# Kernel optimization log

Measured on AMD Instinct MI355X. Metric: run time of the kernel, lower is better.

The kernel has to match this reference:

```python
import jax, jax.numpy as jnp
import numpy as np

N = 1024      # num_waves
L = 32        # latent_dim
H = 64        # hidden_dim
EPS = 1e-6
SELF_SCALE = 0.5
INT_SCALE = 0.3


def _xavier(k, shape, gain=0.5):
    fan_out, fan_in = shape
    std = gain * np.sqrt(2.0 / (fan_in + fan_out))
    return (jax.random.normal(k, shape, jnp.float32) * std).astype(jnp.float32)


def setup_inputs() -> dict:
    key = jax.random.key(0)
    ks = jax.random.split(key, 12)
    d = {}
    d['state'] = jax.random.normal(ks[0], (N * (L + 1),), jnp.float32)
    # SelfDynamicsNetwork: L->H->H->L, tanh, xavier_normal gain=0.5, zero bias
    d['Ws1'] = _xavier(ks[1], (H, L)); d['bs1'] = jnp.zeros((H,), jnp.float32)
    d['Ws2'] = _xavier(ks[2], (H, H)); d['bs2'] = jnp.zeros((H,), jnp.float32)
    d['Ws3'] = _xavier(ks[3], (L, H)); d['bs3'] = jnp.zeros((L,), jnp.float32)
    # InteractionNetwork: 4L->H->H->L
    d['Wi1'] = _xavier(ks[4], (H, 4 * L)); d['bi1'] = jnp.zeros((H,), jnp.float32)
    d['Wi2'] = _xavier(ks[5], (H, H));     d['bi2'] = jnp.zeros((H,), jnp.float32)
    d['Wi3'] = _xavier(ks[6], (L, H));     d['bi3'] = jnp.zeros((L,), jnp.float32)
    # QuantumPhaseMixer
    d['phase_w'] = jax.random.normal(ks[7], (L,), jnp.float32) * 0.1
    d['Wc'] = _xavier(ks[8], (L, 2 * L), gain=1.0)
    d['bc'] = jnp.zeros((L,), jnp.float32)
    # per-wave aggressiveness
    d['aggr'] = jnp.ones((N,), jnp.float32) * 0.5
    return d


def reference(state, Ws1, bs1, Ws2, bs2, Ws3, bs3,
              Wi1, bi1, Wi2, bi2, Wi3, bi3,
              phase_w, Wc, bc, aggr):
    s = state.reshape(N, L + 1)
    h = s[:, :L]          # [N, L]
    phases = s[:, L]      # [N]

    def mlp(x, W1, b1, W2, b2, W3, b3):
        x = jnp.tanh(x @ W1.T + b1)
        x = jnp.tanh(x @ W2.T + b2)
        return x @ W3.T + b3

    self_term = mlp(h, Ws1, bs1, Ws2, bs2, Ws3, bs3)   # [N, L]
    dh = self_term  # prev_state is None -> estimated velocity = self_dynamics(h)

    # pairwise distance factor
    diff = h[:, None, :] - h[None, :, :]                # [N, N, L] (h_i - h_j)
    dist = jnp.linalg.norm(diff, axis=-1) + EPS         # [N, N]
    dfac = jnp.minimum(1.0 / dist, 2.0)

    # InteractionNetwork on concat([h_i, h_j, dh_i, dh_j]): split first layer
    a_i = h @ Wi1[:, :L].T + dh @ Wi1[:, 2 * L:3 * L].T           # [N, H]
    b_j = h @ Wi1[:, L:2 * L].T + dh @ Wi1[:, 3 * L:].T + bi1    # [N, H]
    x1 = jnp.tanh(a_i[:, None, :] + b_j[None, :, :])              # [N, N, H]
    x2 = jnp.tanh(x1 @ Wi2.T + bi2)                               # [N, N, H]
    k_ij = x2 @ Wi3.T + bi3                                       # [N, N, L]

    # QuantumPhaseMixer
    phase_diff = phases[:, None] - phases[None, :]                # [N, N]
    pf = jnp.cos(phase_diff[..., None] * phase_w)                 # [N, N, L]
    coh = jax.nn.sigmoid((h @ Wc[:, :L].T)[:, None, :]
                         + (h @ Wc[:, L:].T)[None, :, :] + bc)    # [N, N, L]
    quantum = pf * coh * (-diff)                                  # h_j - h_i = -diff

    agg = jax.nn.sigmoid(aggr)                                    # [N]
    inter = dfac[..., None] * k_ij * agg[:, None, None] + quantum # [N, N, L]
    mask = 1.0 - jnp.eye(N, dtype=inter.dtype)                    # skip j == i
    isum = jnp.einsum('ijl,ij->il', inter, mask)                  # sum over j

    # env is None -> speed_mults = 1, refractions = 0
    dh_dt = SELF_SCALE * self_term + INT_SCALE * isum
    dphase = 0.1 + 0.05 * jnp.sum(jnp.abs(isum), axis=-1)
    return jnp.concatenate([dh_dt, dphase[:, None]], axis=1).reshape(-1)
```

## Files before the change

### kernel.cpp

```cpp
#include <hip/hip_runtime.h>
#include <hip/hip_bf16.h>
#include <math.h>

#define NN 1024
#define LDIM 32
#define HDIM 64

#define WS_SELF 0
#define WS_AA   (WS_SELF + NN*LDIM)
#define WS_CI   (WS_AA   + NN*HDIM)
#define WS_AGG  (WS_CI   + NN*LDIM)
#define WS_BI2  (WS_AGG  + NN)
#define WS_BI3  (WS_BI2  + HDIM)
#define WS_FEND (WS_BI3  + LDIM)

#define U_BJB  0
#define U_HJB  (U_BJB + NN*HDIM)
#define U_JT   (U_HJB + NN*LDIM)
#define U_W2B  (U_JT  + NN*LDIM*4)
#define U_W3B  (U_W2B + HDIM*HDIM)
#define U_END  (U_W3B + LDIM*HDIM)

#define PK_W1  0
#define PK_W2  1024
#define PK_W3  3072
#define PK_WI1 4096
#define PK_WC  8192
#define PK_END 9216

#define K2P  2.88539008f
#define K1N  (-1.44269504f)

typedef __attribute__((ext_vector_type(8))) short bf16x8;
typedef __attribute__((ext_vector_type(4))) float f32x4;
typedef __attribute__((ext_vector_type(2))) float v2f;

__device__ __forceinline__ float fast_rcp(float x) { return __builtin_amdgcn_rcpf(x); }
__device__ __forceinline__ float fast_tanh(float x) {
    float e = __builtin_amdgcn_exp2f(x * K2P);
    return 1.0f - 2.0f * fast_rcp(e + 1.0f);
}
__device__ __forceinline__ float fast_sigmoid(float x) {
    return fast_rcp(1.0f + __builtin_amdgcn_exp2f(x * K1N));
}
__device__ __forceinline__ float blo(unsigned int u) { union { unsigned int i; float f; } v; v.i = u << 16; return v.f; }
__device__ __forceinline__ float bhi(unsigned int u) { union { unsigned int i; float f; } v; v.i = u & 0xffff0000u; return v.f; }
__device__ __forceinline__ float bf2f(unsigned short u) { union { unsigned int i; float f; } v; v.i = ((unsigned int)u) << 16; return v.f; }
__device__ __forceinline__ unsigned short f2bf(float f) {
    __hip_bfloat16 b = __float2bfloat16(f);
    unsigned short u; __builtin_memcpy(&u, &b, 2); return u;
}
__device__ __forceinline__ unsigned int pk2(float a, float b) {
    float2 t; t.x = a; t.y = b;
    __hip_bfloat162 h = __float22bfloat162_rn(t);
    unsigned int u; __builtin_memcpy(&u, &h, 4); return u;
}

__device__ __forceinline__ v2f tanh2_fact(v2f ea, v2f eb) {
    v2f d = ea * eb + 1.0f;
    v2f r; r.x = fast_rcp(d.x); r.y = fast_rcp(d.y);
    return 1.0f - 2.0f * r;
}

__global__ __launch_bounds__(256) void precompute(
    const float* __restrict__ state,
    const float* __restrict__ Ws1, const float* __restrict__ bs1,
    const float* __restrict__ Ws2, const float* __restrict__ bs2,
    const float* __restrict__ Ws3, const float* __restrict__ bs3,
    const float* __restrict__ Wi1, const float* __restrict__ bi1,
    const float* __restrict__ Wi2, const float* __restrict__ bi2,
    const float* __restrict__ Wi3, const float* __restrict__ bi3,
    const float* __restrict__ phw, const float* __restrict__ Wc,
    const float* __restrict__ bc,  const float* __restrict__ aggr,
    float* __restrict__ ws, unsigned short* __restrict__ wsu) {
    const int tid = threadIdx.x;
    const int w = tid >> 6, t = tid & 63;
    const int i = blockIdx.x * 4 + w;

    __shared__ unsigned int wlds[PK_END];
    __shared__ float shh[4][32], shdh[4][32], sht1[4][64], sht2[4][64];
    __shared__ float shph[4];

    {
        const float2* s1 = (const float2*)Ws1;
        #pragma unroll
        for (int r = 0; r < 4; r++) { int e = tid + r * 256; int f = e >> 4, k2 = e & 15;
            float2 v = s1[e]; wlds[PK_W1 + k2 * 64 + f] = pk2(v.x, v.y); }
        const float2* s2 = (const float2*)Ws2;
        #pragma unroll
        for (int r = 0; r < 8; r++) { int e = tid + r * 256; int f = e >> 5, k2 = e & 31;
            float2 v = s2[e]; wlds[PK_W2 + k2 * 64 + f] = pk2(v.x, v.y); }
        const float2* s3 = (const float2*)Ws3;
        #pragma unroll
        for (int r = 0; r < 4; r++) { int e = tid + r * 256; int f = e >> 5, k2 = e & 31;
            float2 v = s3[e]; wlds[PK_W3 + k2 * 32 + f] = pk2(v.x, v.y); }
        const float2* si = (const float2*)Wi1;
        #pragma unroll
        for (int r = 0; r < 16; r++) { int e = tid + r * 256; int f = e >> 6, c2 = e & 63;
            float2 v = si[e]; wlds[PK_WI1 + c2 * 64 + f] = pk2(v.x, v.y); }
        const float2* sc = (const float2*)Wc;
        #pragma unroll
        for (int r = 0; r < 4; r++) { int e = tid + r * 256; int f = e >> 5, c2 = e & 31;
            float2 v = sc[e]; wlds[PK_WC + c2 * 32 + f] = pk2(v.x, v.y); }
    }
    if (blockIdx.x == 0) {
        #pragma unroll
        for (int r = 0; r < 16; r++) { int e = tid + r * 256; wsu[U_W2B + e] = f2bf(Wi2[e]); }
        #pragma unroll
        for (int r = 0; r < 8; r++)  { int e = tid + r * 256; wsu[U_W3B + e] = f2bf(Wi3[e]); }
        if (tid < HDIM) ws[WS_BI2 + tid] = bi2[tid];
        if (tid < LDIM) ws[WS_BI3 + tid] = bi3[tid];
    }

    float sv = (t < 33) ? state[i * 33 + t] : 0.f;
    if (t < 32) shh[w][t] = sv;
    if (t == 32) shph[w] = sv;
    if (t == 33) ws[WS_AGG + i] = fast_sigmoid(aggr[i]);
    __syncthreads();

    {
        float s = bs1[t];
        const unsigned int* W = wlds + PK_W1;
        #pragma unroll
        for (int k2 = 0; k2 < 16; k2++) {
            unsigned int p = W[k2 * 64 + t];
            s = fmaf(blo(p), shh[w][2 * k2], s);
            s = fmaf(bhi(p), shh[w][2 * k2 + 1], s);
        }
        sht1[w][t] = fast_tanh(s);
    }
    __syncthreads();
    {
        float s = bs2[t];
        const unsigned int* W = wlds + PK_W2;
        #pragma unroll
        for (int k2 = 0; k2 < 32; k2++) {
            unsigned int p = W[k2 * 64 + t];
            s = fmaf(blo(p), sht1[w][2 * k2], s);
            s = fmaf(bhi(p), sht1[w][2 * k2 + 1], s);
        }
        sht2[w][t] = fast_tanh(s);
    }
    __syncthreads();
    if (t < 32) {
        float s = bs3[t];
        const unsigned int* W = wlds + PK_W3;
        #pragma unroll
        for (int k2 = 0; k2 < 32; k2++) {
            unsigned int p = W[k2 * 32 + t];
            s = fmaf(blo(p), sht2[w][2 * k2], s);
            s = fmaf(bhi(p), sht2[w][2 * k2 + 1], s);
        }
        ws[WS_SELF + i * 32 + t] = s;
        shdh[w][t] = s;
    }
    __syncthreads();
    {
        float sa = 0.f, sb = bi1[t];
        const unsigned int* W = wlds + PK_WI1;
        #pragma unroll
        for (int k2 = 0; k2 < 16; k2++) {
            float h0 = shh[w][2 * k2], h1 = shh[w][2 * k2 + 1];
            float d0 = shdh[w][2 * k2], d1 = shdh[w][2 * k2 + 1];
            unsigned int wa  = W[k2 * 64 + t];
            unsigned int wb  = W[(16 + k2) * 64 + t];
            unsigned int wa2 = W[(32 + k2) * 64 + t];
            unsigned int wb2 = W[(48 + k2) * 64 + t];
            sa = fmaf(blo(wa), h0, sa);  sa = fmaf(bhi(wa), h1, sa);
            sb = fmaf(blo(wb), h0, sb);  sb = fmaf(bhi(wb), h1, sb);
            sa = fmaf(blo(wa2), d0, sa); sa = fmaf(bhi(wa2), d1, sa);
            sb = fmaf(blo(wb2), d0, sb); sb = fmaf(bhi(wb2), d1, sb);
        }
        ws[WS_AA + i * 64 + t]  = __builtin_amdgcn_exp2f(sa * K2P);
        wsu[U_BJB + i * 64 + t] = f2bf(__builtin_amdgcn_exp2f(sb * K2P));
    }
    if (t < 32) {
        float si2 = 0.f, sj = 0.f;
        const unsigned int* W = wlds + PK_WC;
        #pragma unroll
        for (int m2 = 0; m2 < 16; m2++) {
            float h0 = shh[w][2 * m2], h1 = shh[w][2 * m2 + 1];
            unsigned int wi = W[m2 * 32 + t];
            unsigned int wj = W[(16 + m2) * 32 + t];
            si2 = fmaf(blo(wi), h0, si2); si2 = fmaf(bhi(wi), h1, si2);
            sj  = fmaf(blo(wj), h0, sj);  sj  = fmaf(bhi(wj), h1, sj);
        }
        ws[WS_CI + i * 32 + t] = __builtin_amdgcn_exp2f((si2 + bc[t]) * K1N);
        float h = shh[w][t];
        wsu[U_HJB + i * 32 + t] = f2bf(h);
        float ejn = __builtin_amdgcn_exp2f(sj * K1N);
        float sc_, cc_;
        __sincosf(shph[w] * phw[t], &sc_, &cc_);
        int p = (t & 15) + 16;
        float h_p  = __shfl(h,   p);
        float e_p  = __shfl(ejn, p);
        float cc_p = __shfl(cc_, p);
        float sc_p = __shfl(sc_, p);
        if (t < 16) {
            uint4 o; o.x = pk2(h, h_p); o.y = pk2(ejn, e_p);
            o.z = pk2(cc_, cc_p); o.w = pk2(sc_, sc_p);
            *(uint4*)(wsu + U_JT + (i * 16 + t) * 8) = o;
        }
    }
}

__global__ __launch_bounds__(256) void pair_kernel(
    const float* __restrict__ ws, const unsigned short* __restrict__ wsu,
    float* __restrict__ out) {
    const int i    = blockIdx.x;
    const int tid  = threadIdx.x;
    const int w    = tid >> 6;
    const int lane = tid & 63;
    const int q    = lane >> 4;
    const int m    = lane & 15;
    const int jw   = w * 16;
    const int sub  = lane & 3;

    __shared__ unsigned short W2ls[64 * 72];
    __shared__ unsigned short x2ls[4 * 16 * 72];
    __shared__ float redT[4][32], redU[4][32], redV[4][32];
    __shared__ float sfw[4];

    {
        int row = tid >> 2, c = (tid & 3) * 16;
        const uint4* s2 = (const uint4*)(wsu + U_W2B + row * 64 + c);
        uint4 d0 = s2[0], d1 = s2[1];
        uint4* dd = (uint4*)(&W2ls[row * 72 + c]);
        dd[0] = d0; dd[1] = d1;
    }
    bf16x8 w3r[2][2];
    #pragma unroll
    for (int lb = 0; lb < 2; lb++)
        #pragma unroll
        for (int s = 0; s < 2; s++)
            w3r[lb][s] = *(const bf16x8*)(wsu + U_W3B + (lb * 16 + m) * 64 + s * 32 + q * 8);

    v2f hi2[4];
    {
        uint4 hv4 = *(const uint4*)(wsu + U_HJB + i * 32 + sub * 8);
        unsigned int hd[4] = {hv4.x, hv4.y, hv4.z, hv4.w};
        #pragma unroll
        for (int e = 0; e < 4; e++) { hi2[e].x = blo(hd[e]); hi2[e].y = bhi(hd[e]); }
    }
    f32x4 b2q[4];
    #pragma unroll
    for (int nb = 0; nb < 4; nb++) {
        float4 bv = *(const float4*)(ws + WS_BI2 + nb * 16 + q * 4);
        b2q[nb][0] = bv.x; b2q[nb][1] = bv.y; b2q[nb][2] = bv.z; b2q[nb][3] = bv.w;
    }
    v2f ea2[8];
    {
        const float* ap = ws + WS_AA + i * 64 + q * 8;
        #pragma unroll
        for (int s = 0; s < 2; s++) {
            float4 lo = *(const float4*)(ap + s * 32);
            float4 hi = *(const float4*)(ap + s * 32 + 4);
            ea2[s * 4 + 0].x = lo.x; ea2[s * 4 + 0].y = lo.y;
            ea2[s * 4 + 1].x = lo.z; ea2[s * 4 + 1].y = lo.w;
            ea2[s * 4 + 2].x = hi.x; ea2[s * 4 + 2].y = hi.y;
            ea2[s * 4 + 3].x = hi.z; ea2[s * 4 + 3].y = hi.w;
        }
    }
    v2f hiv2, ei2;
    hiv2.x = bf2f(wsu[U_HJB + i * 32 + m]);      hiv2.y = bf2f(wsu[U_HJB + i * 32 + 16 + m]);
    ei2.x = ws[WS_CI + i * 32 + m];              ei2.y = ws[WS_CI + i * 32 + 16 + m];
    const float aggi = ws[WS_AGG + i];
    const float sub0 = (sub == 0) ? 1.0f : 0.0f;

    const unsigned short* hp = wsu + U_HJB + (jw + (lane >> 2)) * 32 + sub * 8;
    const unsigned short* bp = wsu + U_BJB + (jw + m) * 64 + q * 8;
    const unsigned short* jp = wsu + U_JT + ((jw + q * 4) * 16 + m) * 8;

    uint4 hvA = *(const uint4*)hp;
    uint4 b0A = *(const uint4*)bp;
    uint4 b1A = *(const uint4*)(bp + 32);
    uint4 hvB, b0B, b1B;
    __syncthreads();

    f32x4 accK[2];
    #pragma unroll
    for (int lb = 0; lb < 2; lb++) { accK[lb][0]=0.f; accK[lb][1]=0.f; accK[lb][2]=0.f; accK[lb][3]=0.f; }
    v2f u2; u2.x = 0.f; u2.y = 0.f;
    v2f vv2; vv2.x = 0.f; vv2.y = 0.f;
    float sumfac = 0.f;

    unsigned short* xb = &x2ls[w * 1152];

    auto stageB = [&]() {
        bf16x8 x2f[2];
        #pragma unroll
        for (int s = 0; s < 2; s++)
            x2f[s] = *(const bf16x8*)(&xb[m * 72 + s * 32 + q * 8]);
        #pragma unroll
        for (int lb = 0; lb < 2; lb++) {
            #pragma unroll
            for (int s = 0; s < 2; s++) {
                accK[lb] = __builtin_amdgcn_mfma_f32_16x16x32_bf16(x2f[s], w3r[lb][s], accK[lb], 0, 0, 0);
            }
        }
    };

    auto body = [&](int T, const uint4& hvc, const uint4& b0c, const uint4& b1c,
                    uint4& hvn, uint4& b0n, uint4& b1n) {
        hp += 2048; bp += 4096;
        hvn = *(const uint4*)hp;
        b0n = *(const uint4*)bp;
        b1n = *(const uint4*)(bp + 32);

        uint4 jt4[4];
        #pragma unroll
        for (int r = 0; r < 4; r++) jt4[r] = *(const uint4*)(jp + r * 128);
        jp += 8192;

        if (T > 0) stageB();

        float facm;
        {
            unsigned int hd[4] = {hvc.x, hvc.y, hvc.z, hvc.w};
            v2f s2v; s2v.x = 0.f; s2v.y = 0.f;
            #pragma unroll
            for (int e = 0; e < 4; e++) {
                v2f hj; hj.x = blo(hd[e]); hj.y = bhi(hd[e]);
                v2f d = hi2[e] - hj;
                s2v += d * d;
            }
            float s = s2v.x + s2v.y;
            s += __shfl_xor(s, 1); s += __shfl_xor(s, 2);
            int jj = T * 64 + jw + (lane >> 2);
            float facown = fminf(__builtin_amdgcn_rsqf(s), 2.0f) * aggi;
            facown = (jj == i) ? 0.0f : facown;
            sumfac = fmaf(sub0, facown, sumfac);
            facm = __shfl(facown, 4 * m);
        }

        bf16x8 afr[2];
        {
            unsigned int bd[8] = {b0c.x, b0c.y, b0c.z, b0c.w, b1c.x, b1c.y, b1c.z, b1c.w};
            #pragma unroll
            for (int s = 0; s < 2; s++) {
                union { uint4 u4; bf16x8 v; } pkd;
                #pragma unroll
                for (int e = 0; e < 4; e++) {
                    unsigned int bw = bd[s * 4 + e];
                    v2f eb; eb.x = blo(bw); eb.y = bhi(bw);
                    v2f t2 = tanh2_fact(ea2[s * 4 + e], eb);
                    ((unsigned int*)&pkd.u4)[e] = pk2(t2.x, t2.y);
                }
                afr[s] = pkd.v;
            }
        }

        f32x4 accA[4];
        #pragma unroll
        for (int nb = 0; nb < 4; nb++) {
            f32x4 acc = b2q[nb];
            #pragma unroll
            for (int s = 0; s < 2; s++) {
                bf16x8 w2f = *(const bf16x8*)(&W2ls[(nb * 16 + m) * 72 + s * 32 + q * 8]);
                acc = __builtin_amdgcn_mfma_f32_16x16x32_bf16(w2f, afr[s], acc, 0, 0, 0);
            }
            accA[nb] = acc;
        }
        #pragma unroll
        for (int nb = 0; nb < 4; nb++) {
            v2f zA; zA.x = accA[nb][0]; zA.y = accA[nb][1];
            v2f zB; zB.x = accA[nb][2]; zB.y = accA[nb][3];
            v2f zzA = zA * zA, zzB = zB * zB;
            v2f nA = zA * (zzA + 15.0f), nB = zB * (zzB + 15.0f);
            v2f dA = zzA * 6.0f + 15.0f, dB = zzB * 6.0f + 15.0f;
            v2f rA, rB;
            rA.x = fast_rcp(dA.x); rA.y = fast_rcp(dA.y);
            rB.x = fast_rcp(dB.x); rB.y = fast_rcp(dB.y);
            v2f tA = nA * (rA * facm);
            v2f tB = nB * (rB * facm);
            uint2 pk; pk.x = pk2(tA.x, tA.y); pk.y = pk2(tB.x, tB.y);
            *(uint2*)(&xb[m * 72 + nb * 16 + q * 4]) = pk;
        }

        #pragma unroll
        for (int r = 0; r < 4; r++) {
            uint4 jv = jt4[r];
            v2f hj2; hj2.x = blo(jv.x); hj2.y = bhi(jv.x);
            v2f ej2; ej2.x = blo(jv.y); ej2.y = bhi(jv.y);
            v2f pc2; pc2.x = blo(jv.z); pc2.y = bhi(jv.z);
            v2f ps2; ps2.x = blo(jv.w); ps2.y = bhi(jv.w);
            v2f dd = ei2 * ej2 + 1.0f;
            v2f coh; coh.x = fast_rcp(dd.x); coh.y = fast_rcp(dd.y);
            v2f cd = coh * (hiv2 - hj2);
            u2  += cd * pc2;
            vv2 += cd * ps2;
        }
    };

    #pragma unroll 1
    for (int T = 0; T < 16; T += 2) {
        body(T,     hvA, b0A, b1A, hvB, b0B, b1B);
        body(T + 1, hvB, b0B, b1B, hvA, b0A, b1A);
    }
    stageB();

    float T1[2];
    float aU[2] = {u2.x, u2.y};
    float aV[2] = {vv2.x, vv2.y};
    #pragma unroll
    for (int lb = 0; lb < 2; lb++) {
        T1[lb] = (accK[lb][0] + accK[lb][1]) + (accK[lb][2] + accK[lb][3]);
        T1[lb] += __shfl_xor(T1[lb], 16); T1[lb] += __shfl_xor(T1[lb], 32);
        aU[lb] += __shfl_xor(aU[lb], 16); aU[lb] += __shfl_xor(aU[lb], 32);
        aV[lb] += __shfl_xor(aV[lb], 16); aV[lb] += __shfl_xor(aV[lb], 32);
    }
    sumfac += __shfl_xor(sumfac, 1);  sumfac += __shfl_xor(sumfac, 2);
    sumfac += __shfl_xor(sumfac, 4);  sumfac += __shfl_xor(sumfac, 8);
    sumfac += __shfl_xor(sumfac, 16); sumfac += __shfl_xor(sumfac, 32);
    if (lane < 16) {
        redT[w][m] = T1[0];      redT[w][16 + m] = T1[1];
        redU[w][m] = aU[0];      redU[w][16 + m] = aU[1];
        redV[w][m] = aV[0];      redV[w][16 + m] = aV[1];
    }
    if (lane == 0) sfw[w] = sumfac;
    __syncthreads();
    if (tid < 32) {
        int l = tid;
        float t1 = (redT[0][l] + redT[1][l]) + (redT[2][l] + redT[3][l]);
        float uu = (redU[0][l] + redU[1][l]) + (redU[2][l] + redU[3][l]);
        float vvv = (redV[0][l] + redV[1][l]) + (redV[2][l] + redV[3][l]);
        float sf = (sfw[0] + sfw[1]) + (sfw[2] + sfw[3]);
        int mm = l & 15;
        uint2 jti = *(const uint2*)(wsu + U_JT + (i * 16 + mm) * 8 + 4);
        float pic = (l < 16) ? blo(jti.x) : bhi(jti.x);
        float pis = (l < 16) ? blo(jti.y) : bhi(jti.y);
        float isum = t1 + sf * ws[WS_BI3 + l] - (pic * uu + pis * vvv);
        out[i * 33 + l] = 0.5f * ws[WS_SELF + i * 32 + l] + 0.3f * isum;
        float ab = fabsf(isum);
        ab += __shfl_xor(ab, 1); ab += __shfl_xor(ab, 2);
        ab += __shfl_xor(ab, 4); ab += __shfl_xor(ab, 8);
        ab += __shfl_xor(ab, 16);
        if (tid == 0) out[i * 33 + 32] = 0.1f + 0.05f * ab;
    }
}

extern "C" void kernel_launch(void* const* d_in, const int* in_sizes, int n_in,
                              void* d_out, int out_size, void* d_ws, size_t ws_size,
                              hipStream_t stream) {
    const float* state   = (const float*)d_in[0];
    const float* Ws1     = (const float*)d_in[1];
    const float* bs1     = (const float*)d_in[2];
    const float* Ws2     = (const float*)d_in[3];
    const float* bs2     = (const float*)d_in[4];
    const float* Ws3     = (const float*)d_in[5];
    const float* bs3     = (const float*)d_in[6];
    const float* Wi1     = (const float*)d_in[7];
    const float* bi1     = (const float*)d_in[8];
    const float* Wi2     = (const float*)d_in[9];
    const float* bi2     = (const float*)d_in[10];
    const float* Wi3     = (const float*)d_in[11];
    const float* bi3     = (const float*)d_in[12];
    const float* phase_w = (const float*)d_in[13];
    const float* Wc      = (const float*)d_in[14];
    const float* bc      = (const float*)d_in[15];
    const float* aggr    = (const float*)d_in[16];

    float* ws = (float*)d_ws;
    unsigned short* wsu = (unsigned short*)(ws + WS_FEND);
    float* out = (float*)d_out;

    precompute<<<256, 256, 0, stream>>>(state, Ws1, bs1, Ws2, bs2, Ws3, bs3,
                                        Wi1, bi1, Wi2, bi2, Wi3, bi3,
                                        phase_w, Wc, bc, aggr, ws, wsu);
    pair_kernel<<<NN, 256, 0, stream>>>(ws, wsu, out);
}
```

Before: 142.2 us.

## Sum scaled x2 over j before applying Wi3 instead of per-pair MFMA

Uses linearity of the last interaction layer. The dfac-scaled tanh outputs x2 are accumulated over j in registers, and Wi3 is applied once per row i at the end. This removes the per-tile LDS staging of x2, the bf16 packing and the second MFMA stage, and adds a cross-lane and cross-wave reduction plus a small scalar dot product in the epilogue. It also keeps the accumulation in fp32 rather than rounding to bf16 before the final matmul.

```diff
diff --git a/kernel.cpp b/kernel.cpp
--- a/kernel.cpp
+++ b/kernel.cpp
@@ -217,8 +217,8 @@
     const int sub  = lane & 3;
 
     __shared__ unsigned short W2ls[64 * 72];
-    __shared__ unsigned short x2ls[4 * 16 * 72];
-    __shared__ float redT[4][32], redU[4][32], redV[4][32];
+    __shared__ float redY[4][64];
+    __shared__ float redU[4][32], redV[4][32];
     __shared__ float sfw[4];
 
     {
@@ -228,12 +228,6 @@
         uint4* dd = (uint4*)(&W2ls[row * 72 + c]);
         dd[0] = d0; dd[1] = d1;
     }
-    bf16x8 w3r[2][2];
-    #pragma unroll
-    for (int lb = 0; lb < 2; lb++)
-        #pragma unroll
-        for (int s = 0; s < 2; s++)
-            w3r[lb][s] = *(const bf16x8*)(wsu + U_W3B + (lb * 16 + m) * 64 + s * 32 + q * 8);
 
     v2f hi2[4];
     {
@@ -277,28 +271,12 @@
     uint4 hvB, b0B, b1B;
     __syncthreads();
 
-    f32x4 accK[2];
+    v2f y2[8];
     #pragma unroll
-    for (int lb = 0; lb < 2; lb++) { accK[lb][0]=0.f; accK[lb][1]=0.f; accK[lb][2]=0.f; accK[lb][3]=0.f; }
+    for (int k = 0; k < 8; k++) { y2[k].x = 0.f; y2[k].y = 0.f; }
     v2f u2; u2.x = 0.f; u2.y = 0.f;
     v2f vv2; vv2.x = 0.f; vv2.y = 0.f;
     float sumfac = 0.f;
-
-    unsigned short* xb = &x2ls[w * 1152];
-
-    auto stageB = [&]() {
-        bf16x8 x2f[2];
-        #pragma unroll
-        for (int s = 0; s < 2; s++)
-            x2f[s] = *(const bf16x8*)(&xb[m * 72 + s * 32 + q * 8]);
-        #pragma unroll
-        for (int lb = 0; lb < 2; lb++) {
-            #pragma unroll
-            for (int s = 0; s < 2; s++) {
-                accK[lb] = __builtin_amdgcn_mfma_f32_16x16x32_bf16(x2f[s], w3r[lb][s], accK[lb], 0, 0, 0);
-            }
-        }
-    };
 
     auto body = [&](int T, const uint4& hvc, const uint4& b0c, const uint4& b1c,
                     uint4& hvn, uint4& b0n, uint4& b1n) {
@@ -311,8 +289,6 @@
         #pragma unroll
         for (int r = 0; r < 4; r++) jt4[r] = *(const uint4*)(jp + r * 128);
         jp += 8192;
-
-        if (T > 0) stageB();
 
         float facm;
         {
@@ -371,10 +347,8 @@
             v2f rA, rB;
             rA.x = fast_rcp(dA.x); rA.y = fast_rcp(dA.y);
             rB.x = fast_rcp(dB.x); rB.y = fast_rcp(dB.y);
-            v2f tA = nA * (rA * facm);
-            v2f tB = nB * (rB * facm);
-            uint2 pk; pk.x = pk2(tA.x, tA.y); pk.y = pk2(tB.x, tB.y);
-            *(uint2*)(&xb[m * 72 + nb * 16 + q * 4]) = pk;
+            y2[nb * 2 + 0] += nA * (rA * facm);
+            y2[nb * 2 + 1] += nB * (rB * facm);
         }
 
         #pragma unroll
@@ -397,15 +371,30 @@
         body(T,     hvA, b0A, b1A, hvB, b0B, b1B);
         body(T + 1, hvB, b0B, b1B, hvA, b0A, b1A);
     }
-    stageB();
-
-    float T1[2];
+
+    float yv[16];
+    #pragma unroll
+    for (int nb = 0; nb < 4; nb++) {
+        yv[nb * 4 + 0] = y2[nb * 2 + 0].x; yv[nb * 4 + 1] = y2[nb * 2 + 0].y;
+        yv[nb * 4 + 2] = y2[nb * 2 + 1].x; yv[nb * 4 + 3] = y2[nb * 2 + 1].y;
+    }
+    #pragma unroll
+    for (int k = 0; k < 16; k++) {
+        yv[k] += __shfl_xor(yv[k], 1); yv[k] += __shfl_xor(yv[k], 2);
+        yv[k] += __shfl_xor(yv[k], 4); yv[k] += __shfl_xor(yv[k], 8);
+    }
+    if (m == 0) {
+        #pragma unroll
+        for (int nb = 0; nb < 4; nb++) {
+            #pragma unroll
+            for (int e = 0; e < 4; e++)
+                redY[w][nb * 16 + q * 4 + e] = yv[nb * 4 + e];
+        }
+    }
     float aU[2] = {u2.x, u2.y};
     float aV[2] = {vv2.x, vv2.y};
     #pragma unroll
     for (int lb = 0; lb < 2; lb++) {
-        T1[lb] = (accK[lb][0] + accK[lb][1]) + (accK[lb][2] + accK[lb][3]);
-        T1[lb] += __shfl_xor(T1[lb], 16); T1[lb] += __shfl_xor(T1[lb], 32);
         aU[lb] += __shfl_xor(aU[lb], 16); aU[lb] += __shfl_xor(aU[lb], 32);
         aV[lb] += __shfl_xor(aV[lb], 16); aV[lb] += __shfl_xor(aV[lb], 32);
     }
@@ -413,15 +402,30 @@
     sumfac += __shfl_xor(sumfac, 4);  sumfac += __shfl_xor(sumfac, 8);
     sumfac += __shfl_xor(sumfac, 16); sumfac += __shfl_xor(sumfac, 32);
     if (lane < 16) {
-        redT[w][m] = T1[0];      redT[w][16 + m] = T1[1];
         redU[w][m] = aU[0];      redU[w][16 + m] = aU[1];
         redV[w][m] = aV[0];      redV[w][16 + m] = aV[1];
     }
     if (lane == 0) sfw[w] = sumfac;
     __syncthreads();
+    if (tid < 64) {
+        redY[0][tid] = (redY[0][tid] + redY[1][tid]) + (redY[2][tid] + redY[3][tid]);
+    }
+    __syncthreads();
     if (tid < 32) {
         int l = tid;
-        float t1 = (redT[0][l] + redT[1][l]) + (redT[2][l] + redT[3][l]);
+        float t1 = 0.f;
+        const uint4* w3p = (const uint4*)(wsu + U_W3B + l * 64);
+        #pragma unroll
+        for (int c = 0; c < 8; c++) {
+            uint4 wv = w3p[c];
+            unsigned int wd[4] = {wv.x, wv.y, wv.z, wv.w};
+            const float* yp = &redY[0][c * 8];
+            #pragma unroll
+            for (int e = 0; e < 4; e++) {
+                t1 = fmaf(blo(wd[e]), yp[2 * e],     t1);
+                t1 = fmaf(bhi(wd[e]), yp[2 * e + 1], t1);
+            }
+        }
         float uu = (redU[0][l] + redU[1][l]) + (redU[2][l] + redU[3][l]);
         float vvv = (redV[0][l] + redV[1][l]) + (redV[2][l] + redV[3][l]);
         float sf = (sfw[0] + sfw[1]) + (sfw[2] + sfw[3]);
```

New measurement: 138.6 us. 2.6% less time.
